# Kernel tuning notes

Measured on AMD Instinct MI355X. Metric: run time of the kernel, lower is better.

Reference implementation:

```python
import jax, jax.numpy as jnp
import numpy as np
from functools import partial

DIM = 256
HEADS = 8
HEAD_DIM = DIM // HEADS
SCALES = (1, 2, 4)
B, H, W = 1, 64, 64


def _dwconv3x3(x, w, b):
    # x: (B,C,H,W), w: (C,1,3,3) depthwise, b: (C,)
    y = jax.lax.conv_general_dilated(
        x, w, window_strides=(1, 1), padding='SAME',
        feature_group_count=x.shape[1],
        dimension_numbers=('NCHW', 'OIHW', 'NCHW'))
    return y + b[None, :, None, None]


def _pwconv(x, w, b):
    # 1x1 conv: x (B,C,H,W), w (O,C), b (O,)
    return jnp.einsum('bchw,oc->bohw', x, w) + b[None, :, None, None]


def _avg_pool(x, s):
    Bb, C, Hh, Ww = x.shape
    return x.reshape(Bb, C, Hh // s, s, Ww // s, s).mean(axis=(3, 5))


def setup_inputs() -> dict:
    key = jax.random.key(0)
    ks = jax.random.split(key, 9)
    sc = 0.05
    return {
        'x': jax.random.normal(ks[0], (B, DIM, H, W), dtype=jnp.float32),
        'dw_w': jax.random.normal(ks[1], (3, DIM, 1, 3, 3), dtype=jnp.float32) * sc,
        'dw_b': jax.random.normal(ks[2], (3, DIM), dtype=jnp.float32) * sc,
        'pw_w': jax.random.normal(ks[3], (3, 3 * DIM, DIM), dtype=jnp.float32) * sc,
        'pw_b': jax.random.normal(ks[4], (3, 3 * DIM), dtype=jnp.float32) * sc,
        'pos_w': jax.random.normal(ks[5], (3, DIM, 1, 3, 3), dtype=jnp.float32) * sc,
        'pos_b': jax.random.normal(ks[6], (3, DIM), dtype=jnp.float32) * sc,
        'fusion_w': jax.random.normal(ks[7], (DIM, 3 * DIM), dtype=jnp.float32) * sc,
        'fusion_b': jax.random.normal(ks[8], (DIM,), dtype=jnp.float32) * sc,
    }


def reference(x, dw_w, dw_b, pw_w, pw_b, pos_w, pos_b, fusion_w, fusion_b):
    Bb, C, Hh, Ww = x.shape
    outputs = []
    for i, scale in enumerate(SCALES):
        xs = _avg_pool(x, scale) if scale > 1 else x
        # ConvQKV
        x_dw = _dwconv3x3(xs, dw_w[i], dw_b[i])
        qkv = _pwconv(x_dw, pw_w[i], pw_b[i])
        q, k, v = jnp.split(qkv, 3, axis=1)
        pos = _dwconv3x3(xs, pos_w[i], pos_b[i])
        q = q + pos
        k = k + pos
        Hs, Ws = xs.shape[2], xs.shape[3]
        Ns = Hs * Ws
        # (B, heads, head_dim, N)
        q = q.reshape(Bb, HEADS, HEAD_DIM, Ns)
        k = k.reshape(Bb, HEADS, HEAD_DIM, Ns)
        v = v.reshape(Bb, HEADS, HEAD_DIM, Ns)
        attn = jnp.einsum('bhdn,bhdm->bhnm', q, k) / (HEAD_DIM ** 0.5)
        attn = jax.nn.softmax(attn, axis=-1)
        out = jnp.einsum('bhnm,bhdm->bhdn', attn, v)  # (B,h,hd,N)
        out = out.reshape(Bb, C, Hs, Ws)
        if scale > 1:
            out = jax.image.resize(out, (Bb, C, Hh, Ww), method='bilinear')
        outputs.append(out)
    cat = jnp.concatenate(outputs, axis=1)  # (B, 3C, H, W)
    return jnp.einsum('bchw,oc->bohw', cat, fusion_w) + fusion_b[None, :, None, None]
```

## Files before the change

### kernel.cpp

```cpp
#include <hip/hip_runtime.h>
#include <math.h>

#define DIM 256
#define HEADS 8
#define HD 32
#define QSCALE 0.25504526770295183f

typedef __attribute__((ext_vector_type(8))) short bf16x8;
typedef __attribute__((ext_vector_type(4))) float f32x4;

#if __has_builtin(__builtin_amdgcn_exp2f)
#define EXP2(x) __builtin_amdgcn_exp2f(x)
#else
#define EXP2(x) __expf((x) * 0.6931471805599453f)
#endif

__device__ __forceinline__ unsigned short f2bf(float f) {
  unsigned int u = __float_as_uint(f);
  unsigned int r = u + 0x7fff + ((u >> 16) & 1);
  return (unsigned short)(r >> 16);
}
__device__ __forceinline__ float bf2f(unsigned short u) {
  return __uint_as_float(((unsigned int)u) << 16);
}

__global__ __launch_bounds__(256) void prep_kernel(const float* __restrict__ x,
    const float* __restrict__ pw_w, const float* __restrict__ fus_w,
    float* __restrict__ xs2, float* __restrict__ xs4,
    unsigned short* __restrict__ Wb, unsigned short* __restrict__ Wf) {
  const int gx = blockIdx.x, t = threadIdx.x;
  if (gx < 1024) {
    int id = gx * 256 + t;
    int c = id >> 10, n = id & 1023;
    int y = (n >> 5) << 1, x0 = (n & 31) << 1;
    const float* b = x + c * 4096 + y * 64 + x0;
    xs2[id] = (b[0] + b[1] + b[64] + b[65]) * 0.25f;
  } else if (gx < 1280) {
    int id = (gx - 1024) * 256 + t;
    int c = id >> 8, n = id & 255;
    int y = (n >> 4) << 2, x0 = (n & 15) << 2;
    const float* b = x + c * 4096 + y * 64 + x0;
    float s = 0.f;
    #pragma unroll
    for (int dy = 0; dy < 4; ++dy)
      #pragma unroll
      for (int dx = 0; dx < 4; ++dx) s += b[dy * 64 + dx];
    xs4[id] = s * 0.0625f;
  } else if (gx < 1856) {
    int id = (gx - 1280) * 256 + t;
    float4 v = *(const float4*)(pw_w + id * 4);
    ushort4 st; st.x = f2bf(v.x); st.y = f2bf(v.y); st.z = f2bf(v.z); st.w = f2bf(v.w);
    *(ushort4*)(Wb + id * 4) = st;
  } else {
    int id = (gx - 1856) * 256 + t;
    float4 v = *(const float4*)(fus_w + id * 4);
    ushort4 st; st.x = f2bf(v.x); st.y = f2bf(v.y); st.z = f2bf(v.z); st.w = f2bf(v.w);
    *(ushort4*)(Wf + id * 4) = st;
  }
}

__global__ __launch_bounds__(256) void dwt_kernel(const float* __restrict__ x,
    const float* __restrict__ xs2, const float* __restrict__ xs4,
    const float* __restrict__ dw_w, const float* __restrict__ dw_b,
    const float* __restrict__ pos_w, const float* __restrict__ pos_b,
    unsigned short* __restrict__ xdwT, unsigned short* __restrict__ posT) {
  __shared__ unsigned short lds1[64][72];
  __shared__ unsigned short lds2[64][72];
  int b = blockIdx.x;
  const float* src;
  int lgHs, wo, soff, c0, n0;
  if (b < 256)      { src = x;   lgHs = 6; wo = 0; soff = 0;
                      c0 = (b >> 6) * 64; n0 = (b & 63) * 64; }
  else if (b < 320) { b -= 256; src = xs2; lgHs = 5; wo = 1; soff = 1048576;
                      c0 = (b >> 4) * 64; n0 = (b & 15) * 64; }
  else              { b -= 320; src = xs4; lgHs = 4; wo = 2; soff = 1310720;
                      c0 = (b >> 2) * 64; n0 = (b & 3) * 64; }
  const int Hs = 1 << lgHs;
  const int Ns = Hs * Hs;
  const int t = threadIdx.x;
  #pragma unroll
  for (int p = 0; p < 4; ++p) {
    int cl = p * 16 + (t >> 4);
    int c = c0 + cl;
    const float* w1 = dw_w + wo * 2304 + c * 9;
    const float* w2 = pos_w + wo * 2304 + c * 9;
    float b1 = dw_b[wo * 256 + c], b2 = pos_b[wo * 256 + c];
    int nb = (t & 15) * 4;
    int gn = n0 + nb;
    int y = gn >> lgHs, xg = gn & (Hs - 1);
    const float* sc = src + c * Ns;
    float r[3][6];
    #pragma unroll
    for (int ky = 0; ky < 3; ++ky) {
      int yy = y + ky - 1;
      bool rok = (yy >= 0) && (yy < Hs);
      #pragma unroll
      for (int j = 0; j < 6; ++j) {
        int xx = xg - 1 + j;
        r[ky][j] = (rok && xx >= 0 && xx < Hs) ? sc[yy * Hs + xx] : 0.f;
      }
    }
    #pragma unroll
    for (int i = 0; i < 4; ++i) {
      float s1 = b1, s2 = b2;
      #pragma unroll
      for (int ky = 0; ky < 3; ++ky)
        #pragma unroll
        for (int kx = 0; kx < 3; ++kx) {
          float v = r[ky][i + kx];
          s1 += v * w1[ky * 3 + kx];
          s2 += v * w2[ky * 3 + kx];
        }
      lds1[nb + i][cl] = f2bf(s1);
      lds2[nb + i][cl] = f2bf(s2);
    }
  }
  __syncthreads();
  int n = t >> 2, seg = (t & 3) * 16;
  size_t o = (size_t)soff + (size_t)(n0 + n) * 256 + c0 + seg;
  *(bf16x8*)(xdwT + o)     = *(const bf16x8*)&lds1[n][seg];
  *(bf16x8*)(xdwT + o + 8) = *(const bf16x8*)&lds1[n][seg + 8];
  *(bf16x8*)(posT + o)     = *(const bf16x8*)&lds2[n][seg];
  *(bf16x8*)(posT + o + 8) = *(const bf16x8*)&lds2[n][seg + 8];
}

__global__ __launch_bounds__(256) void gemm_qkv_all(const unsigned short* __restrict__ WbA,
    const unsigned short* __restrict__ xdwTA, const float* __restrict__ biasA,
    const unsigned short* __restrict__ posTA, unsigned short* __restrict__ Qf,
    unsigned short* __restrict__ Kf, unsigned short* __restrict__ Vf) {
  int by = blockIdx.y;
  int Ns, off;
  const unsigned short *Wb, *xdwT, *posT;
  const float* bias;
  if (by < 64) {
    Ns = 4096; off = 0;
    Wb = WbA; bias = biasA;
  } else if (by < 80) {
    Ns = 1024; off = 1048576; by -= 64;
    Wb = WbA + 196608; bias = biasA + 768;
  } else {
    Ns = 256; off = 1310720; by -= 80;
    Wb = WbA + 393216; bias = biasA + 1536;
  }
  xdwT = xdwTA + off; posT = posTA + off;
  const int t = threadIdx.x;
  const int wave = t >> 6, lane = t & 63;
  const int ln = lane & 15, quad = lane >> 4;
  const int o0 = blockIdx.x * 64 + (wave & 1) * 32;
  const int n0 = by * 64 + (wave >> 1) * 32;
  const unsigned short* a0 = Wb + (size_t)(o0 + ln) * 256 + quad * 8;
  const unsigned short* a1 = a0 + 16 * 256;
  const unsigned short* b0 = xdwT + (size_t)(n0 + ln) * 256 + quad * 8;
  const unsigned short* b1 = b0 + 16 * 256;
  f32x4 acc[2][2] = {};
  #pragma unroll
  for (int ks = 0; ks < 8; ++ks) {
    bf16x8 af0 = *(const bf16x8*)(a0 + ks * 32);
    bf16x8 af1 = *(const bf16x8*)(a1 + ks * 32);
    bf16x8 bv0 = *(const bf16x8*)(b0 + ks * 32);
    bf16x8 bv1 = *(const bf16x8*)(b1 + ks * 32);
    acc[0][0] = __builtin_amdgcn_mfma_f32_16x16x32_bf16(af0, bv0, acc[0][0], 0, 0, 0);
    acc[0][1] = __builtin_amdgcn_mfma_f32_16x16x32_bf16(af0, bv1, acc[0][1], 0, 0, 0);
    acc[1][0] = __builtin_amdgcn_mfma_f32_16x16x32_bf16(af1, bv0, acc[1][0], 0, 0, 0);
    acc[1][1] = __builtin_amdgcn_mfma_f32_16x16x32_bf16(af1, bv1, acc[1][1], 0, 0, 0);
  }
  const int cat = blockIdx.x >> 2;
  #pragma unroll
  for (int mt = 0; mt < 2; ++mt) {
    int ot = o0 + mt * 16 + quad * 4;
    float bs0 = bias[ot], bs1 = bias[ot + 1], bs2 = bias[ot + 2], bs3 = bias[ot + 3];
    #pragma unroll
    for (int nt = 0; nt < 2; ++nt) {
      int nn = n0 + nt * 16 + ln;
      f32x4 v = acc[mt][nt];
      v.x += bs0; v.y += bs1; v.z += bs2; v.w += bs3;
      if (cat < 2) {
        int c = ot & 255;
        ushort4 p4 = *(const ushort4*)(posT + (size_t)nn * 256 + c);
        v.x += bf2f(p4.x); v.y += bf2f(p4.y); v.z += bf2f(p4.z); v.w += bf2f(p4.w);
        if (cat == 0) { v.x *= QSCALE; v.y *= QSCALE; v.z *= QSCALE; v.w *= QSCALE; }
        ushort4 st;
        st.x = f2bf(v.x); st.y = f2bf(v.y); st.z = f2bf(v.z); st.w = f2bf(v.w);
        int hh = c >> 5, d = c & 31;
        unsigned short* dst = (cat == 0 ? Qf : Kf) + off;
        size_t a = ((size_t)(hh * (Ns >> 4) + (nn >> 4)) * 64 + (d >> 3) * 16 + (nn & 15)) * 8
                   + (d & 7);
        *(ushort4*)(dst + a) = st;
      } else {
        int c = ot - 512;
        int hh = c >> 5, d = c & 31;
        int dt = d >> 4, lnv = d & 15;
        size_t a = ((((size_t)hh * (Ns >> 5) + (nn >> 5)) * 2 + dt) * 64
                    + ((nn & 31) >> 3) * 16) * 8 + (nn & 7);
        unsigned short* dst = Vf + off;
        dst[a + (size_t)(lnv + 0) * 8] = f2bf(v.x);
        dst[a + (size_t)(lnv + 1) * 8] = f2bf(v.y);
        dst[a + (size_t)(lnv + 2) * 8] = f2bf(v.z);
        dst[a + (size_t)(lnv + 3) * 8] = f2bf(v.w);
      }
    }
  }
}

__global__ __launch_bounds__(256) void attn_all_kernel(
    const unsigned short* __restrict__ Qf, const unsigned short* __restrict__ Kf,
    const unsigned short* __restrict__ Vf,
    unsigned short* __restrict__ accp1, unsigned short* __restrict__ p2,
    unsigned short* __restrict__ p4, float* __restrict__ ls1,
    float* __restrict__ ls2, float* __restrict__ ls4) {
  __shared__ unsigned short pt_lds[4 * 32 * 72];
  const int z = blockIdx.z;
  unsigned short* accp;
  float* lsump;
  int Ns, lgMs, sp, off;
  if (z < 8) {
    accp = accp1; lsump = ls1; Ns = 4096; lgMs = 9; sp = z; off = 0;
  } else if (z < 16) {
    if (blockIdx.x >= 8) return;
    accp = p2; lsump = ls2; Ns = 1024; lgMs = 7; sp = z - 8; off = 1048576;
  } else {
    if (blockIdx.x >= 2) return;
    accp = p4; lsump = ls4; Ns = 256; lgMs = 6; sp = z - 16; off = 1310720;
  }
  const int t = threadIdx.x;
  const int wave = t >> 6, lane = t & 63;
  const int ln = lane & 15, quad = lane >> 4;
  const int h = blockIdx.y;
  const int n0 = blockIdx.x * 128 + wave * 32;
  const unsigned short* qp = Qf + off
      + ((size_t)(h * (Ns >> 4) + (n0 >> 4)) * 64 + lane) * 8;
  bf16x8 qf0 = *(const bf16x8*)(qp);
  bf16x8 qf1 = *(const bf16x8*)(qp + 512);
  unsigned short* ptw = pt_lds + wave * (32 * 72);
  f32x4 acc[2][2] = {};
  f32x4 acc_l0 = {0.f, 0.f, 0.f, 0.f}, acc_l1 = {0.f, 0.f, 0.f, 0.f};
  const f32x4 zero = {0.f, 0.f, 0.f, 0.f};
  const short kOne = (short)0x3F80;
  const bf16x8 onesf = {kOne, kOne, kOne, kOne, kOne, kOne, kOne, kOne};
  const int m0s = sp << lgMs;
  const int nch = 1 << (lgMs - 6);
  const unsigned short* kp = Kf + off
      + ((size_t)(h * (Ns >> 4) + (m0s >> 4)) * 64 + lane) * 8;
  const unsigned short* vp = Vf + off
      + (((size_t)h * (Ns >> 5) + (m0s >> 5)) * 128 + lane) * 8;
  for (int ch = 0; ch < nch; ++ch) {
    const unsigned short* kc = kp + ch * 2048;
    const unsigned short* vc = vp + ch * 2048;
    bf16x8 kf0 = *(const bf16x8*)(kc);
    bf16x8 kf1 = *(const bf16x8*)(kc + 512);
    bf16x8 kf2 = *(const bf16x8*)(kc + 1024);
    bf16x8 kf3 = *(const bf16x8*)(kc + 1536);
    bf16x8 vf00 = *(const bf16x8*)(vc);
    bf16x8 vf10 = *(const bf16x8*)(vc + 512);
    bf16x8 vf01 = *(const bf16x8*)(vc + 1024);
    bf16x8 vf11 = *(const bf16x8*)(vc + 1536);
    f32x4 s[4][2];
    s[0][0] = __builtin_amdgcn_mfma_f32_16x16x32_bf16(kf0, qf0, zero, 0, 0, 0);
    s[0][1] = __builtin_amdgcn_mfma_f32_16x16x32_bf16(kf0, qf1, zero, 0, 0, 0);
    s[1][0] = __builtin_amdgcn_mfma_f32_16x16x32_bf16(kf1, qf0, zero, 0, 0, 0);
    s[1][1] = __builtin_amdgcn_mfma_f32_16x16x32_bf16(kf1, qf1, zero, 0, 0, 0);
    s[2][0] = __builtin_amdgcn_mfma_f32_16x16x32_bf16(kf2, qf0, zero, 0, 0, 0);
    s[2][1] = __builtin_amdgcn_mfma_f32_16x16x32_bf16(kf2, qf1, zero, 0, 0, 0);
    s[3][0] = __builtin_amdgcn_mfma_f32_16x16x32_bf16(kf3, qf0, zero, 0, 0, 0);
    s[3][1] = __builtin_amdgcn_mfma_f32_16x16x32_bf16(kf3, qf1, zero, 0, 0, 0);
    #pragma unroll
    for (int mt = 0; mt < 4; ++mt) {
      #pragma unroll
      for (int nt = 0; nt < 2; ++nt) {
        float e0 = EXP2(s[mt][nt].x);
        float e1 = EXP2(s[mt][nt].y);
        float e2 = EXP2(s[mt][nt].z);
        float e3 = EXP2(s[mt][nt].w);
        uint2 pk;
        pk.x = __builtin_amdgcn_perm(__float_as_uint(e1), __float_as_uint(e0), 0x07060302);
        pk.y = __builtin_amdgcn_perm(__float_as_uint(e3), __float_as_uint(e2), 0x07060302);
        *(uint2*)&ptw[(nt * 16 + ln) * 72 + mt * 16 + quad * 4] = pk;
      }
    }
    #pragma unroll
    for (int ks = 0; ks < 2; ++ks) {
      bf16x8 pf0 = *(const bf16x8*)&ptw[ln * 72 + ks * 32 + quad * 8];
      bf16x8 pf1 = *(const bf16x8*)&ptw[(16 + ln) * 72 + ks * 32 + quad * 8];
      bf16x8 va = ks ? vf01 : vf00;
      bf16x8 vbf = ks ? vf11 : vf10;
      acc[0][0] = __builtin_amdgcn_mfma_f32_16x16x32_bf16(va, pf0, acc[0][0], 0, 0, 0);
      acc[0][1] = __builtin_amdgcn_mfma_f32_16x16x32_bf16(va, pf1, acc[0][1], 0, 0, 0);
      acc[1][0] = __builtin_amdgcn_mfma_f32_16x16x32_bf16(vbf, pf0, acc[1][0], 0, 0, 0);
      acc[1][1] = __builtin_amdgcn_mfma_f32_16x16x32_bf16(vbf, pf1, acc[1][1], 0, 0, 0);
      acc_l0 = __builtin_amdgcn_mfma_f32_16x16x32_bf16(onesf, pf0, acc_l0, 0, 0, 0);
      acc_l1 = __builtin_amdgcn_mfma_f32_16x16x32_bf16(onesf, pf1, acc_l1, 0, 0, 0);
    }
  }
  unsigned short* ap = accp + ((size_t)sp * 256 + h * 32) * Ns;
  #pragma unroll
  for (int dt = 0; dt < 2; ++dt) {
    #pragma unroll
    for (int r = 0; r < 4; ++r) {
      int cl = dt * 16 + quad * 4 + r;
      ap[(size_t)cl * Ns + n0 + ln]      = f2bf(((const float*)&acc[dt][0])[r]);
      ap[(size_t)cl * Ns + n0 + 16 + ln] = f2bf(((const float*)&acc[dt][1])[r]);
    }
  }
  if (lane < 16) {
    float* lp = lsump + ((size_t)sp * 8 + h) * Ns + n0;
    lp[lane]      = acc_l0.x;
    lp[16 + lane] = acc_l1.x;
  }
}

__global__ __launch_bounds__(256) void combine24_kernel(const unsigned short* __restrict__ p2,
    const float* __restrict__ ls2, const unsigned short* __restrict__ p4,
    const float* __restrict__ ls4, float* __restrict__ out2, float* __restrict__ out4) {
  int id = blockIdx.x * 256 + threadIdx.x;
  if (id < 262144) {
    int n = id & 1023, h = id >> 15;
    float v = 0.f, d = 0.f;
    #pragma unroll
    for (int sp = 0; sp < 8; ++sp) {
      v += bf2f(p2[sp * 262144 + id]);
      d += ls2[sp * 8192 + h * 1024 + n];
    }
    out2[id] = v / d;
  } else {
    int idl = id - 262144;
    int n = idl & 255, h = idl >> 13;
    float v = 0.f, d = 0.f;
    #pragma unroll
    for (int sp = 0; sp < 4; ++sp) {
      v += bf2f(p4[sp * 65536 + idl]);
      d += ls4[sp * 2048 + h * 256 + n];
    }
    out4[idl] = v / d;
  }
}

__global__ __launch_bounds__(256) void build_catT_kernel(const unsigned short* __restrict__ accp,
    const float* __restrict__ lsum1, const float* __restrict__ out2,
    const float* __restrict__ out4, unsigned short* __restrict__ catT) {
  __shared__ unsigned short lds[64][72];
  const int t = threadIdx.x;
  const int n0 = blockIdx.x * 64;
  const int by = blockIdx.y;
  const int c0 = by * 64;
  if (by < 4) {
    #pragma unroll
    for (int p = 0; p < 4; ++p) {
      int ct = p * 16 + (t >> 4);
      int c = c0 + ct;
      int h = c >> 5;
      int nn = (t & 15) * 4;
      float vs[4] = {0.f, 0.f, 0.f, 0.f};
      float ds[4] = {0.f, 0.f, 0.f, 0.f};
      #pragma unroll
      for (int sp = 0; sp < 8; ++sp) {
        ushort4 a = *(const ushort4*)(accp + (size_t)sp * 1048576 + (size_t)c * 4096 + n0 + nn);
        vs[0] += bf2f(a.x); vs[1] += bf2f(a.y); vs[2] += bf2f(a.z); vs[3] += bf2f(a.w);
        float4 dd = *(const float4*)(lsum1 + (size_t)sp * 32768 + (size_t)h * 4096 + n0 + nn);
        ds[0] += dd.x; ds[1] += dd.y; ds[2] += dd.z; ds[3] += dd.w;
      }
      lds[nn + 0][ct] = f2bf(vs[0] / ds[0]);
      lds[nn + 1][ct] = f2bf(vs[1] / ds[1]);
      lds[nn + 2][ct] = f2bf(vs[2] / ds[2]);
      lds[nn + 3][ct] = f2bf(vs[3] / ds[3]);
    }
  } else {
    const bool s2 = by < 8;
    const float* src = s2 ? out2 : out4;
    const int Hs = s2 ? 32 : 16;
    const int coff = s2 ? 256 : 512;
    const float sc = (float)Hs / 64.0f;
    #pragma unroll
    for (int p = 0; p < 4; ++p) {
      int ct = p * 16 + (t >> 4);
      const float* s = src + (size_t)(c0 - coff + ct) * Hs * Hs;
      int nn = (t & 15) * 4;
      #pragma unroll
      for (int i = 0; i < 4; ++i) {
        int n = n0 + nn + i;
        int y = n >> 6, x = n & 63;
        float fy = ((float)y + 0.5f) * sc - 0.5f;
        float fx = ((float)x + 0.5f) * sc - 0.5f;
        float fy0 = floorf(fy), fx0 = floorf(fx);
        int y0 = (int)fy0, x0 = (int)fx0;
        float ty = fy - fy0, tx = fx - fx0;
        int y0c = min(max(y0, 0), Hs - 1), y1c = min(max(y0 + 1, 0), Hs - 1);
        int x0c = min(max(x0, 0), Hs - 1), x1c = min(max(x0 + 1, 0), Hs - 1);
        float v00 = s[y0c * Hs + x0c], v01 = s[y0c * Hs + x1c];
        float v10 = s[y1c * Hs + x0c], v11 = s[y1c * Hs + x1c];
        float v0 = v00 + (v01 - v00) * tx;
        float v1 = v10 + (v11 - v10) * tx;
        lds[nn + i][ct] = f2bf(v0 + (v1 - v0) * ty);
      }
    }
  }
  __syncthreads();
  int n = t >> 2, seg = (t & 3) * 16;
  *(bf16x8*)(catT + (size_t)(n0 + n) * 768 + c0 + seg)     = *(const bf16x8*)&lds[n][seg];
  *(bf16x8*)(catT + (size_t)(n0 + n) * 768 + c0 + seg + 8) = *(const bf16x8*)&lds[n][seg + 8];
}

__global__ __launch_bounds__(256) void gemm_fus_mfma(const unsigned short* __restrict__ Wf,
    const unsigned short* __restrict__ catT, float* __restrict__ part) {
  const int t = threadIdx.x;
  const int wave = t >> 6, lane = t & 63;
  const int ln = lane & 15, quad = lane >> 4;
  const int o0 = blockIdx.x * 64 + (wave & 1) * 32;
  const int n0 = blockIdx.y * 64 + (wave >> 1) * 32;
  const int sp = blockIdx.z;
  const int k0 = sp * 256;
  const unsigned short* a0 = Wf + (size_t)(o0 + ln) * 768 + k0 + quad * 8;
  const unsigned short* a1 = a0 + 16 * 768;
  const unsigned short* b0 = catT + (size_t)(n0 + ln) * 768 + k0 + quad * 8;
  const unsigned short* b1 = b0 + 16 * 768;
  f32x4 acc[2][2] = {};
  #pragma unroll
  for (int ks = 0; ks < 8; ++ks) {
    bf16x8 af0 = *(const bf16x8*)(a0 + ks * 32);
    bf16x8 af1 = *(const bf16x8*)(a1 + ks * 32);
    bf16x8 bv0 = *(const bf16x8*)(b0 + ks * 32);
    bf16x8 bv1 = *(const bf16x8*)(b1 + ks * 32);
    acc[0][0] = __builtin_amdgcn_mfma_f32_16x16x32_bf16(af0, bv0, acc[0][0], 0, 0, 0);
    acc[0][1] = __builtin_amdgcn_mfma_f32_16x16x32_bf16(af0, bv1, acc[0][1], 0, 0, 0);
    acc[1][0] = __builtin_amdgcn_mfma_f32_16x16x32_bf16(af1, bv0, acc[1][0], 0, 0, 0);
    acc[1][1] = __builtin_amdgcn_mfma_f32_16x16x32_bf16(af1, bv1, acc[1][1], 0, 0, 0);
  }
  float* pp = part + (size_t)sp * 1048576;
  #pragma unroll
  for (int mt = 0; mt < 2; ++mt) {
    #pragma unroll
    for (int nt = 0; nt < 2; ++nt) {
      #pragma unroll
      for (int r = 0; r < 4; ++r) {
        pp[(size_t)(o0 + mt * 16 + quad * 4 + r) * 4096 + n0 + nt * 16 + ln] =
            ((const float*)&acc[mt][nt])[r];
      }
    }
  }
}

__global__ __launch_bounds__(256) void fus_combine_kernel(const float* __restrict__ part,
    const float* __restrict__ bias, float* __restrict__ out) {
  int id = blockIdx.x * 256 + threadIdx.x;
  int o = id >> 10;
  float4 v0 = *(const float4*)(part + id * 4);
  float4 v1 = *(const float4*)(part + 1048576 + id * 4);
  float4 v2 = *(const float4*)(part + 2097152 + id * 4);
  float bs = bias[o];
  float4 r;
  r.x = v0.x + v1.x + v2.x + bs;
  r.y = v0.y + v1.y + v2.y + bs;
  r.z = v0.z + v1.z + v2.z + bs;
  r.w = v0.w + v1.w + v2.w + bs;
  *(float4*)(out + id * 4) = r;
}

extern "C" void kernel_launch(void* const* d_in, const int* in_sizes, int n_in,
                              void* d_out, int out_size, void* d_ws, size_t ws_size,
                              hipStream_t stream) {
  const float* x     = (const float*)d_in[0];
  const float* dw_w  = (const float*)d_in[1];
  const float* dw_b  = (const float*)d_in[2];
  const float* pw_w  = (const float*)d_in[3];
  const float* pw_b  = (const float*)d_in[4];
  const float* pos_w = (const float*)d_in[5];
  const float* pos_b = (const float*)d_in[6];
  const float* fus_w = (const float*)d_in[7];
  const float* fus_b = (const float*)d_in[8];
  float* out = (float*)d_out;
  float* ws = (float*)d_ws;

  float* scratch = ws;
  float* posF   = ws + 1376256;
  float* accpF  = ws + 2752512;
  unsigned short* xdwT = (unsigned short*)(ws + 6946816);
  unsigned short* posT = (unsigned short*)(ws + 7634944);
  unsigned short* Qf   = (unsigned short*)(ws + 8323072);
  unsigned short* Kf   = Qf + 1376256;
  unsigned short* Vf   = (unsigned short*)(ws + 9699328);
  unsigned short* catT = (unsigned short*)(ws + 10387456);
  unsigned short* Wf   = (unsigned short*)(ws + 11960320);

  float* xs2 = accpF;
  float* xs4 = accpF + 262144;
  unsigned short* Wb = catT;
  unsigned short* accp = (unsigned short*)accpF;
  float* lsump1 = posF;
  float* lsump2 = posF + 262144;
  float* lsump4 = posF + 327680;
  float* out2   = posF + 335872;
  float* out4   = posF + 598016;
  unsigned short* p2 = (unsigned short*)scratch;
  unsigned short* p4 = (unsigned short*)scratch + 2097152;
  float* part = accpF;

  prep_kernel<<<2048, 256, 0, stream>>>(x, pw_w, fus_w, xs2, xs4, Wb, Wf);
  dwt_kernel<<<336, 256, 0, stream>>>(x, xs2, xs4, dw_w, dw_b, pos_w, pos_b, xdwT, posT);
  gemm_qkv_all<<<dim3(12, 84), 256, 0, stream>>>(Wb, xdwT, pw_b, posT, Qf, Kf, Vf);

  attn_all_kernel<<<dim3(32, 8, 20), 256, 0, stream>>>(Qf, Kf, Vf, accp, p2, p4,
                                                       lsump1, lsump2, lsump4);
  combine24_kernel<<<1280, 256, 0, stream>>>(p2, lsump2, p4, lsump4, out2, out4);

  build_catT_kernel<<<dim3(64, 12), 256, 0, stream>>>(accp, lsump1, out2, out4, catT);
  gemm_fus_mfma<<<dim3(4, 64, 3), 256, 0, stream>>>(Wf, catT, part);
  fus_combine_kernel<<<1024, 256, 0, stream>>>(part, fus_b, out);
}
```

Before: 170.9 us.

## Pre-tile GEMM operands into MFMA fragment layout for contiguous loads

Weights, depthwise outputs and the concat buffer are now written in a tiled layout where each 16x32 MFMA fragment is a contiguous 512-element block, so every GEMM lane loads 16 contiguous bytes at stride lane*8 instead of strided rows. For the V blocks and the fusion GEMM, the MFMA operands are swapped so that results come out transposed, allowing vectorized ushort4/float4 stores in place of scalar scattered stores. The dwt kernel is retiled to 32-position blocks with twice as many blocks. This adds index complexity in the prep, dwt and catT builders, and the gains are limited because these GEMMs are a small share of the total time.

```diff
diff --git a/kernel.cpp b/kernel.cpp
--- a/kernel.cpp
+++ b/kernel.cpp
@@ -23,6 +23,7 @@
 __device__ __forceinline__ float bf2f(unsigned short u) {
   return __uint_as_float(((unsigned int)u) << 16);
 }
+
 
 __global__ __launch_bounds__(256) void prep_kernel(const float* __restrict__ x,
     const float* __restrict__ pw_w, const float* __restrict__ fus_w,
@@ -46,16 +47,47 @@
       #pragma unroll
       for (int dx = 0; dx < 4; ++dx) s += b[dy * 64 + dx];
     xs4[id] = s * 0.0625f;
-  } else if (gx < 1856) {
-    int id = (gx - 1280) * 256 + t;
-    float4 v = *(const float4*)(pw_w + id * 4);
-    ushort4 st; st.x = f2bf(v.x); st.y = f2bf(v.y); st.z = f2bf(v.z); st.w = f2bf(v.w);
-    *(ushort4*)(Wb + id * 4) = st;
-  } else {
-    int id = (gx - 1856) * 256 + t;
-    float4 v = *(const float4*)(fus_w + id * 4);
-    ushort4 st; st.x = f2bf(v.x); st.y = f2bf(v.y); st.z = f2bf(v.z); st.w = f2bf(v.w);
-    *(ushort4*)(Wf + id * 4) = st;
+  } else if (gx < 1424) {
+    int lid = (gx - 1280) * 256 + t;
+    int fb = lid >> 5, l = lid & 31;
+    int scale = fb / 384, bs = fb - scale * 384;
+    int rtile = bs >> 3, kchunk = bs & 7;
+    int r = scale * 768 + rtile * 16 + (l & 7) * 2;
+    int k = kchunk * 32 + (l >> 3) * 8;
+    const float* s0 = pw_w + (size_t)r * 256 + k;
+    float4 u0 = *(const float4*)(s0);
+    float4 u1 = *(const float4*)(s0 + 4);
+    float4 u2 = *(const float4*)(s0 + 256);
+    float4 u3 = *(const float4*)(s0 + 260);
+    unsigned short* d = Wb + (size_t)fb * 512 + l * 16;
+    ushort4 a0 = {f2bf(u0.x), f2bf(u0.y), f2bf(u0.z), f2bf(u0.w)};
+    ushort4 a1 = {f2bf(u1.x), f2bf(u1.y), f2bf(u1.z), f2bf(u1.w)};
+    ushort4 a2 = {f2bf(u2.x), f2bf(u2.y), f2bf(u2.z), f2bf(u2.w)};
+    ushort4 a3 = {f2bf(u3.x), f2bf(u3.y), f2bf(u3.z), f2bf(u3.w)};
+    *(ushort4*)(d)      = a0;
+    *(ushort4*)(d + 4)  = a1;
+    *(ushort4*)(d + 8)  = a2;
+    *(ushort4*)(d + 12) = a3;
+  } else {
+    int lid = (gx - 1424) * 256 + t;
+    int fb = lid >> 5, l = lid & 31;
+    int rtile = fb / 24, kchunk = fb - rtile * 24;
+    int r = rtile * 16 + (l & 7) * 2;
+    int k = kchunk * 32 + (l >> 3) * 8;
+    const float* s0 = fus_w + (size_t)r * 768 + k;
+    float4 u0 = *(const float4*)(s0);
+    float4 u1 = *(const float4*)(s0 + 4);
+    float4 u2 = *(const float4*)(s0 + 768);
+    float4 u3 = *(const float4*)(s0 + 772);
+    unsigned short* d = Wf + (size_t)fb * 512 + l * 16;
+    ushort4 a0 = {f2bf(u0.x), f2bf(u0.y), f2bf(u0.z), f2bf(u0.w)};
+    ushort4 a1 = {f2bf(u1.x), f2bf(u1.y), f2bf(u1.z), f2bf(u1.w)};
+    ushort4 a2 = {f2bf(u2.x), f2bf(u2.y), f2bf(u2.z), f2bf(u2.w)};
+    ushort4 a3 = {f2bf(u3.x), f2bf(u3.y), f2bf(u3.z), f2bf(u3.w)};
+    *(ushort4*)(d)      = a0;
+    *(ushort4*)(d + 4)  = a1;
+    *(ushort4*)(d + 8)  = a2;
+    *(ushort4*)(d + 12) = a3;
   }
 }
 
@@ -64,28 +96,27 @@
     const float* __restrict__ dw_w, const float* __restrict__ dw_b,
     const float* __restrict__ pos_w, const float* __restrict__ pos_b,
     unsigned short* __restrict__ xdwT, unsigned short* __restrict__ posT) {
-  __shared__ unsigned short lds1[64][72];
-  __shared__ unsigned short lds2[64][72];
+  __shared__ unsigned short lds1[32][72];
+  __shared__ unsigned short lds2[32][72];
   int b = blockIdx.x;
   const float* src;
-  int lgHs, wo, soff, c0, n0;
-  if (b < 256)      { src = x;   lgHs = 6; wo = 0; soff = 0;
-                      c0 = (b >> 6) * 64; n0 = (b & 63) * 64; }
-  else if (b < 320) { b -= 256; src = xs2; lgHs = 5; wo = 1; soff = 1048576;
-                      c0 = (b >> 4) * 64; n0 = (b & 15) * 64; }
-  else              { b -= 320; src = xs4; lgHs = 4; wo = 2; soff = 1310720;
-                      c0 = (b >> 2) * 64; n0 = (b & 3) * 64; }
+  int lgHs, wo, soff;
+  if (b < 512)      { src = x;   lgHs = 6; wo = 0; soff = 0; }
+  else if (b < 640) { b -= 512; src = xs2; lgHs = 5; wo = 1; soff = 1048576; }
+  else              { b -= 640; src = xs4; lgHs = 4; wo = 2; soff = 1310720; }
+  const int c0 = (b & 3) * 64;
+  const int n0 = (b >> 2) * 32;
   const int Hs = 1 << lgHs;
   const int Ns = Hs * Hs;
   const int t = threadIdx.x;
   #pragma unroll
-  for (int p = 0; p < 4; ++p) {
-    int cl = p * 16 + (t >> 4);
+  for (int p = 0; p < 2; ++p) {
+    int cl = p * 32 + (t >> 3);
     int c = c0 + cl;
     const float* w1 = dw_w + wo * 2304 + c * 9;
     const float* w2 = pos_w + wo * 2304 + c * 9;
     float b1 = dw_b[wo * 256 + c], b2 = pos_b[wo * 256 + c];
-    int nb = (t & 15) * 4;
+    int nb = (t & 7) * 4;
     int gn = n0 + nb;
     int y = gn >> lgHs, xg = gn & (Hs - 1);
     const float* sc = src + c * Ns;
@@ -116,12 +147,19 @@
     }
   }
   __syncthreads();
-  int n = t >> 2, seg = (t & 3) * 16;
-  size_t o = (size_t)soff + (size_t)(n0 + n) * 256 + c0 + seg;
-  *(bf16x8*)(xdwT + o)     = *(const bf16x8*)&lds1[n][seg];
-  *(bf16x8*)(xdwT + o + 8) = *(const bf16x8*)&lds1[n][seg + 8];
-  *(bf16x8*)(posT + o)     = *(const bf16x8*)&lds2[n][seg];
-  *(bf16x8*)(posT + o + 8) = *(const bf16x8*)&lds2[n][seg + 8];
+  {
+    int blk = t >> 6, l = t & 63;
+    int ntile = blk >> 1, cchunk = blk & 1;
+    int koct = l >> 4, rr = l & 15;
+    size_t bid = (size_t)((n0 >> 4) + ntile) * 8 + (c0 >> 5) + cchunk;
+    *(bf16x8*)(xdwT + soff + bid * 512 + (size_t)l * 8) =
+        *(const bf16x8*)&lds1[ntile * 16 + rr][cchunk * 32 + koct * 8];
+  }
+  {
+    int n = t >> 3, cseg = (t & 7) * 8;
+    *(bf16x8*)(posT + soff + (size_t)(n0 + n) * 256 + c0 + cseg) =
+        *(const bf16x8*)&lds2[n][cseg];
+  }
 }
 
 __global__ __launch_bounds__(256) void gemm_qkv_all(const unsigned short* __restrict__ WbA,
@@ -148,33 +186,46 @@
   const int ln = lane & 15, quad = lane >> 4;
   const int o0 = blockIdx.x * 64 + (wave & 1) * 32;
   const int n0 = by * 64 + (wave >> 1) * 32;
-  const unsigned short* a0 = Wb + (size_t)(o0 + ln) * 256 + quad * 8;
-  const unsigned short* a1 = a0 + 16 * 256;
-  const unsigned short* b0 = xdwT + (size_t)(n0 + ln) * 256 + quad * 8;
-  const unsigned short* b1 = b0 + 16 * 256;
+  const int at0 = (o0 >> 4) * 8, at1 = at0 + 8;
+  const int bt0 = (n0 >> 4) * 8, bt1 = bt0 + 8;
+  const bool vblk = blockIdx.x >= 8;
   f32x4 acc[2][2] = {};
-  #pragma unroll
-  for (int ks = 0; ks < 8; ++ks) {
-    bf16x8 af0 = *(const bf16x8*)(a0 + ks * 32);
-    bf16x8 af1 = *(const bf16x8*)(a1 + ks * 32);
-    bf16x8 bv0 = *(const bf16x8*)(b0 + ks * 32);
-    bf16x8 bv1 = *(const bf16x8*)(b1 + ks * 32);
-    acc[0][0] = __builtin_amdgcn_mfma_f32_16x16x32_bf16(af0, bv0, acc[0][0], 0, 0, 0);
-    acc[0][1] = __builtin_amdgcn_mfma_f32_16x16x32_bf16(af0, bv1, acc[0][1], 0, 0, 0);
-    acc[1][0] = __builtin_amdgcn_mfma_f32_16x16x32_bf16(af1, bv0, acc[1][0], 0, 0, 0);
-    acc[1][1] = __builtin_amdgcn_mfma_f32_16x16x32_bf16(af1, bv1, acc[1][1], 0, 0, 0);
-  }
-  const int cat = blockIdx.x >> 2;
-  #pragma unroll
-  for (int mt = 0; mt < 2; ++mt) {
-    int ot = o0 + mt * 16 + quad * 4;
-    float bs0 = bias[ot], bs1 = bias[ot + 1], bs2 = bias[ot + 2], bs3 = bias[ot + 3];
-    #pragma unroll
-    for (int nt = 0; nt < 2; ++nt) {
-      int nn = n0 + nt * 16 + ln;
-      f32x4 v = acc[mt][nt];
-      v.x += bs0; v.y += bs1; v.z += bs2; v.w += bs3;
-      if (cat < 2) {
+  if (!vblk) {
+    #pragma unroll
+    for (int ks = 0; ks < 8; ++ks) {
+      bf16x8 af0 = *(const bf16x8*)(Wb + (size_t)(at0 + ks) * 512 + lane * 8);
+      bf16x8 af1 = *(const bf16x8*)(Wb + (size_t)(at1 + ks) * 512 + lane * 8);
+      bf16x8 bv0 = *(const bf16x8*)(xdwT + (size_t)(bt0 + ks) * 512 + lane * 8);
+      bf16x8 bv1 = *(const bf16x8*)(xdwT + (size_t)(bt1 + ks) * 512 + lane * 8);
+      acc[0][0] = __builtin_amdgcn_mfma_f32_16x16x32_bf16(af0, bv0, acc[0][0], 0, 0, 0);
+      acc[0][1] = __builtin_amdgcn_mfma_f32_16x16x32_bf16(af0, bv1, acc[0][1], 0, 0, 0);
+      acc[1][0] = __builtin_amdgcn_mfma_f32_16x16x32_bf16(af1, bv0, acc[1][0], 0, 0, 0);
+      acc[1][1] = __builtin_amdgcn_mfma_f32_16x16x32_bf16(af1, bv1, acc[1][1], 0, 0, 0);
+    }
+  } else {
+    #pragma unroll
+    for (int ks = 0; ks < 8; ++ks) {
+      bf16x8 af0 = *(const bf16x8*)(Wb + (size_t)(at0 + ks) * 512 + lane * 8);
+      bf16x8 af1 = *(const bf16x8*)(Wb + (size_t)(at1 + ks) * 512 + lane * 8);
+      bf16x8 bv0 = *(const bf16x8*)(xdwT + (size_t)(bt0 + ks) * 512 + lane * 8);
+      bf16x8 bv1 = *(const bf16x8*)(xdwT + (size_t)(bt1 + ks) * 512 + lane * 8);
+      acc[0][0] = __builtin_amdgcn_mfma_f32_16x16x32_bf16(bv0, af0, acc[0][0], 0, 0, 0);
+      acc[0][1] = __builtin_amdgcn_mfma_f32_16x16x32_bf16(bv0, af1, acc[0][1], 0, 0, 0);
+      acc[1][0] = __builtin_amdgcn_mfma_f32_16x16x32_bf16(bv1, af0, acc[1][0], 0, 0, 0);
+      acc[1][1] = __builtin_amdgcn_mfma_f32_16x16x32_bf16(bv1, af1, acc[1][1], 0, 0, 0);
+    }
+  }
+  if (!vblk) {
+    const int cat = blockIdx.x >> 2;
+    #pragma unroll
+    for (int mt = 0; mt < 2; ++mt) {
+      int ot = o0 + mt * 16 + quad * 4;
+      float bs0 = bias[ot], bs1 = bias[ot + 1], bs2 = bias[ot + 2], bs3 = bias[ot + 3];
+      #pragma unroll
+      for (int nt = 0; nt < 2; ++nt) {
+        int nn = n0 + nt * 16 + ln;
+        f32x4 v = acc[mt][nt];
+        v.x += bs0; v.y += bs1; v.z += bs2; v.w += bs3;
         int c = ot & 255;
         ushort4 p4 = *(const ushort4*)(posT + (size_t)nn * 256 + c);
         v.x += bf2f(p4.x); v.y += bf2f(p4.y); v.z += bf2f(p4.z); v.w += bf2f(p4.w);
@@ -186,17 +237,26 @@
         size_t a = ((size_t)(hh * (Ns >> 4) + (nn >> 4)) * 64 + (d >> 3) * 16 + (nn & 15)) * 8
                    + (d & 7);
         *(ushort4*)(dst + a) = st;
-      } else {
-        int c = ot - 512;
+      }
+    }
+  } else {
+    #pragma unroll
+    for (int a = 0; a < 2; ++a) {
+      int nbase = n0 + a * 16 + quad * 4;
+      #pragma unroll
+      for (int bb = 0; bb < 2; ++bb) {
+        int o = o0 + bb * 16 + ln;
+        int c = o - 512;
         int hh = c >> 5, d = c & 31;
-        int dt = d >> 4, lnv = d & 15;
-        size_t a = ((((size_t)hh * (Ns >> 5) + (nn >> 5)) * 2 + dt) * 64
-                    + ((nn & 31) >> 3) * 16) * 8 + (nn & 7);
-        unsigned short* dst = Vf + off;
-        dst[a + (size_t)(lnv + 0) * 8] = f2bf(v.x);
-        dst[a + (size_t)(lnv + 1) * 8] = f2bf(v.y);
-        dst[a + (size_t)(lnv + 2) * 8] = f2bf(v.z);
-        dst[a + (size_t)(lnv + 3) * 8] = f2bf(v.w);
+        int dt = d >> 4, dl = d & 15;
+        float bs = bias[o];
+        f32x4 v = acc[a][bb];
+        ushort4 st;
+        st.x = f2bf(v.x + bs); st.y = f2bf(v.y + bs);
+        st.z = f2bf(v.z + bs); st.w = f2bf(v.w + bs);
+        size_t adr = ((((size_t)hh * (Ns >> 5) + (nbase >> 5)) * 2 + dt) * 64
+                      + ((nbase & 31) >> 3) * 16 + dl) * 8 + (nbase & 7);
+        *(ushort4*)(Vf + off + adr) = st;
       }
     }
   }
@@ -394,9 +454,13 @@
     }
   }
   __syncthreads();
-  int n = t >> 2, seg = (t & 3) * 16;
-  *(bf16x8*)(catT + (size_t)(n0 + n) * 768 + c0 + seg)     = *(const bf16x8*)&lds[n][seg];
-  *(bf16x8*)(catT + (size_t)(n0 + n) * 768 + c0 + seg + 8) = *(const bf16x8*)&lds[n][seg + 8];
+  int blk = t >> 5, l = t & 31;
+  int ntile = blk >> 1, cchunk = blk & 1;
+  int koct = l >> 3, r1 = (l & 7) * 2;
+  size_t bid = (size_t)((n0 >> 4) + ntile) * 24 + (c0 >> 5) + cchunk;
+  unsigned short* dst = catT + bid * 512 + (size_t)l * 16;
+  *(bf16x8*)(dst)     = *(const bf16x8*)&lds[ntile * 16 + r1][cchunk * 32 + koct * 8];
+  *(bf16x8*)(dst + 8) = *(const bf16x8*)&lds[ntile * 16 + r1 + 1][cchunk * 32 + koct * 8];
 }
 
 __global__ __launch_bounds__(256) void gemm_fus_mfma(const unsigned short* __restrict__ Wf,
@@ -407,33 +471,30 @@
   const int o0 = blockIdx.x * 64 + (wave & 1) * 32;
   const int n0 = blockIdx.y * 64 + (wave >> 1) * 32;
   const int sp = blockIdx.z;
-  const int k0 = sp * 256;
-  const unsigned short* a0 = Wf + (size_t)(o0 + ln) * 768 + k0 + quad * 8;
-  const unsigned short* a1 = a0 + 16 * 768;
-  const unsigned short* b0 = catT + (size_t)(n0 + ln) * 768 + k0 + quad * 8;
-  const unsigned short* b1 = b0 + 16 * 768;
+  const int at0 = (o0 >> 4) * 24 + sp * 8, at1 = at0 + 24;
+  const int bt0 = (n0 >> 4) * 24 + sp * 8, bt1 = bt0 + 24;
   f32x4 acc[2][2] = {};
   #pragma unroll
   for (int ks = 0; ks < 8; ++ks) {
-    bf16x8 af0 = *(const bf16x8*)(a0 + ks * 32);
-    bf16x8 af1 = *(const bf16x8*)(a1 + ks * 32);
-    bf16x8 bv0 = *(const bf16x8*)(b0 + ks * 32);
-    bf16x8 bv1 = *(const bf16x8*)(b1 + ks * 32);
-    acc[0][0] = __builtin_amdgcn_mfma_f32_16x16x32_bf16(af0, bv0, acc[0][0], 0, 0, 0);
-    acc[0][1] = __builtin_amdgcn_mfma_f32_16x16x32_bf16(af0, bv1, acc[0][1], 0, 0, 0);
-    acc[1][0] = __builtin_amdgcn_mfma_f32_16x16x32_bf16(af1, bv0, acc[1][0], 0, 0, 0);
-    acc[1][1] = __builtin_amdgcn_mfma_f32_16x16x32_bf16(af1, bv1, acc[1][1], 0, 0, 0);
+    bf16x8 af0 = *(const bf16x8*)(Wf + (size_t)(at0 + ks) * 512 + lane * 8);
+    bf16x8 af1 = *(const bf16x8*)(Wf + (size_t)(at1 + ks) * 512 + lane * 8);
+    bf16x8 bv0 = *(const bf16x8*)(catT + (size_t)(bt0 + ks) * 512 + lane * 8);
+    bf16x8 bv1 = *(const bf16x8*)(catT + (size_t)(bt1 + ks) * 512 + lane * 8);
+    acc[0][0] = __builtin_amdgcn_mfma_f32_16x16x32_bf16(bv0, af0, acc[0][0], 0, 0, 0);
+    acc[0][1] = __builtin_amdgcn_mfma_f32_16x16x32_bf16(bv0, af1, acc[0][1], 0, 0, 0);
+    acc[1][0] = __builtin_amdgcn_mfma_f32_16x16x32_bf16(bv1, af0, acc[1][0], 0, 0, 0);
+    acc[1][1] = __builtin_amdgcn_mfma_f32_16x16x32_bf16(bv1, af1, acc[1][1], 0, 0, 0);
   }
   float* pp = part + (size_t)sp * 1048576;
   #pragma unroll
-  for (int mt = 0; mt < 2; ++mt) {
-    #pragma unroll
-    for (int nt = 0; nt < 2; ++nt) {
-      #pragma unroll
-      for (int r = 0; r < 4; ++r) {
-        pp[(size_t)(o0 + mt * 16 + quad * 4 + r) * 4096 + n0 + nt * 16 + ln] =
-            ((const float*)&acc[mt][nt])[r];
-      }
+  for (int a = 0; a < 2; ++a) {
+    int nbase = n0 + a * 16 + quad * 4;
+    #pragma unroll
+    for (int bb = 0; bb < 2; ++bb) {
+      int o = o0 + bb * 16 + ln;
+      float4 st;
+      st.x = acc[a][bb].x; st.y = acc[a][bb].y; st.z = acc[a][bb].z; st.w = acc[a][bb].w;
+      *(float4*)(pp + (size_t)o * 4096 + nbase) = st;
     }
   }
 }
@@ -493,8 +554,8 @@
   unsigned short* p4 = (unsigned short*)scratch + 2097152;
   float* part = accpF;
 
-  prep_kernel<<<2048, 256, 0, stream>>>(x, pw_w, fus_w, xs2, xs4, Wb, Wf);
-  dwt_kernel<<<336, 256, 0, stream>>>(x, xs2, xs4, dw_w, dw_b, pos_w, pos_b, xdwT, posT);
+  prep_kernel<<<1472, 256, 0, stream>>>(x, pw_w, fus_w, xs2, xs4, Wb, Wf);
+  dwt_kernel<<<672, 256, 0, stream>>>(x, xs2, xs4, dw_w, dw_b, pos_w, pos_b, xdwT, posT);
   gemm_qkv_all<<<dim3(12, 84), 256, 0, stream>>>(Wb, xdwT, pw_b, posT, Qf, Kf, Vf);
 
   attn_all_kernel<<<dim3(32, 8, 20), 256, 0, stream>>>(Qf, Kf, Vf, accp, p2, p4,
```

Result: faster. 150.7 us (-11.8%).
